# Kernel tuning notes

Hardware: AMD Instinct MI355X
Metric: run time of the kernel (lower is better)

Reference implementation:

```python
import jax, jax.numpy as jnp
import numpy as np

B, S, E = 4, 2048, 512
H, D = 8, 64  # n_head, attn_dim


def setup_inputs() -> dict:
    key = jax.random.key(0)
    ks = jax.random.split(key, 12)
    scale = 0.02
    return {
        "input_q": jax.random.normal(ks[0], (B, S, E), dtype=jnp.float32),
        "input_k": jax.random.normal(ks[1], (B, S, E), dtype=jnp.float32),
        "input_v": jax.random.normal(ks[2], (B, S, E), dtype=jnp.float32),
        "mask": jax.random.randint(ks[3], (B, S, S), 0, 2, dtype=jnp.int32),
        "wq": jax.random.normal(ks[4], (E, H * D), dtype=jnp.float32) * scale,
        "bq": jnp.zeros((H * D,), dtype=jnp.float32),
        "wk": jax.random.normal(ks[5], (E, H * D), dtype=jnp.float32) * scale,
        "bk": jnp.zeros((H * D,), dtype=jnp.float32),
        "wv": jax.random.normal(ks[6], (E, H * D), dtype=jnp.float32) * scale,
        "bv": jnp.zeros((H * D,), dtype=jnp.float32),
        "wo": jax.random.normal(ks[7], (H * D, E), dtype=jnp.float32) * scale,
        "bo": jnp.zeros((E,), dtype=jnp.float32),
    }


def reference(input_q, input_k, input_v, mask, wq, bq, wk, bk, wv, bv, wo, bo):
    b, lq, _ = input_q.shape
    lk = input_k.shape[1]
    # projections -> [b, len, H, D] -> [b, H, len, D]
    q = (input_q @ wq + bq).reshape(b, lq, H, D).transpose(0, 2, 1, 3)
    k = (input_k @ wk + bk).reshape(b, lk, H, D).transpose(0, 2, 1, 3)
    v = (input_v @ wv + bv).reshape(b, lk, H, D).transpose(0, 2, 1, 3)
    # raw scores [b, H, lq, lk]
    score = jnp.einsum("bhqd,bhkd->bhqk", q, k)
    # NOTE: original masks with -1e9 BEFORE dividing by sqrt(attn_dim)
    score = jnp.where(mask[:, None, :, :] == 0, jnp.float32(-1e9), score)
    attn = jax.nn.softmax(score / jnp.sqrt(jnp.float32(D)), axis=-1)
    out = jnp.einsum("bhqk,bhkd->bqhd", attn, v).reshape(b, lq, H * D)
    return out @ wo + bo
```

## Files before the change

kernel.cpp:

```cpp
#include <hip/hip_runtime.h>
#include <hip/hip_bf16.h>
#include <hip/hip_fp16.h>
#include <stdint.h>

#define Bc 4
#define Sc 2048
#define Ec 512
#define Hc 8
#define Dc 64
#define HDc 512

typedef __attribute__((ext_vector_type(8))) short bf16x8;
typedef __attribute__((ext_vector_type(4))) _Float16 f16x4;
typedef __attribute__((ext_vector_type(8))) _Float16 f16x8;
typedef __attribute__((ext_vector_type(4))) float f32x4;
typedef unsigned int u32;

__device__ __forceinline__ unsigned short f2bf(float x) {
    union { float f; unsigned u; } v; v.f = x;
    unsigned r = v.u + 0x7FFFu + ((v.u >> 16) & 1u);
    return (unsigned short)(r >> 16);
}

__device__ __forceinline__ unsigned pkbf2(float a, float b) {
    float2 f; f.x = a; f.y = b;
    __hip_bfloat162 h = __float22bfloat162_rn(f);
    union { __hip_bfloat162 h2; unsigned u; } u; u.h2 = h;
    return u.u;
}

__device__ __forceinline__ unsigned short f2h(float x) {
    return __half_as_ushort(__float2half_rn(x));
}

__device__ __forceinline__ unsigned pkh2(float a, float b) {
    union { __half2 h2; unsigned u; } u;
    u.h2 = __floats2half2_rn(a, b);
    return u.u;
}

__device__ __forceinline__ uint4 pack8(float4 a, float4 b) {
    uint4 v;
    v.x = pkbf2(a.x, a.y); v.y = pkbf2(a.z, a.w);
    v.z = pkbf2(b.x, b.y); v.w = pkbf2(b.z, b.w);
    return v;
}

__device__ __forceinline__ void gload_lds(const void* g, void* l) {
    __builtin_amdgcn_global_load_lds(
        (const __attribute__((address_space(1))) u32*)g,
        (__attribute__((address_space(3))) u32*)l,
        16, 0, 0);
}

__device__ __forceinline__ int vperm(int mt, int c) {
    return ((c >> 2) << 4) + ((mt >> 1) << 3) + ((mt & 1) << 2) + (c & 3);
}

__global__ __launch_bounds__(256) void prep(
    const int* __restrict__ mask, unsigned long long* __restrict__ bits,
    const float* __restrict__ W0, const float* __restrict__ W1,
    const float* __restrict__ W2, const float* __restrict__ W3,
    unsigned short* __restrict__ Wt,
    const float* __restrict__ Xq, const float* __restrict__ Xk,
    const float* __restrict__ Xv, unsigned short* __restrict__ Xb)
{
    const int blk = blockIdx.x;
    __shared__ float t[64][65];
    if (blk < 256) {
        const int z = blk >> 6;
        const float* W = z == 0 ? W0 : (z == 1 ? W1 : (z == 2 ? W2 : W3));
        unsigned short* O = Wt + (size_t)z * Ec * HDc;
        const int k0 = ((blk >> 3) & 7) * 64, n0 = (blk & 7) * 64;
#pragma unroll
        for (int i = 0; i < 16; i++) {
            int idx = threadIdx.x + 256 * i;
            int kr = idx >> 6, nc = idx & 63;
            t[nc][kr] = W[(size_t)(k0 + kr) * HDc + n0 + nc];
        }
        __syncthreads();
#pragma unroll
        for (int i = 0; i < 16; i++) {
            int idx = threadIdx.x + 256 * i;
            int nr = idx >> 6, kc = idx & 63;
            O[(size_t)(n0 + nr) * Ec + k0 + kc] = f2bf(t[nr][kc]);
        }
    } else if (blk < 2304) {
        const int lane = threadIdx.x & 63;
        int wave = ((blk - 256) * 256 + (int)threadIdx.x) >> 6;
        const int nwaves = (2048 * 256) >> 6;
        const int nwords = (Bc * Sc * Sc) / 64;
        for (int w = wave; w < nwords; w += nwaves) {
            int m = mask[(size_t)w * 64 + lane];
            unsigned long long b = __ballot(m != 0);
            if (lane == 0) bits[w] = b;
        }
    } else {
        const int zi = blk - 2304;
        const int z = zi >> 11, wi = zi & 2047;
        const float* X = z == 0 ? Xq : (z == 1 ? Xk : Xv);
        const size_t off = ((size_t)wi * 256 + threadIdx.x) * 8;
        const float4* p = (const float4*)(X + off);
        float4 f0 = p[0], f1 = p[1];
        *(uint4*)(Xb + (size_t)z * 4194304 + off) = pack8(f0, f1);
    }
}

__global__ __launch_bounds__(256) void proj_gemm(
    const unsigned short* __restrict__ Xb, const unsigned short* __restrict__ Wt,
    const float* __restrict__ bq, const float* __restrict__ bk, const float* __restrict__ bv,
    unsigned short* __restrict__ Oq, unsigned short* __restrict__ Ok,
    unsigned short* __restrict__ Vt)
{
    const int z = blockIdx.z;
    const unsigned short* Xz = Xb + (size_t)z * 4194304;
    const unsigned short* Bt = Wt + (size_t)z * Ec * HDc;
    const float* bias = z == 0 ? bq : (z == 1 ? bk : bv);

    const int n0 = blockIdx.x * 128;
    const int m0 = blockIdx.y * 128;
    const int tid = threadIdx.x, lane = tid & 63, w = tid >> 6;
    const int c = lane & 15, quad = lane >> 4;
    const int wm = w & 1, wn = w >> 1;

    __shared__ unsigned short As[128 * 64];
    __shared__ unsigned short Bs[128 * 64];

    f32x4 acc[4][4];
#pragma unroll
    for (int i = 0; i < 4; i++)
#pragma unroll
        for (int j = 0; j < 4; j++) acc[i][j] = (f32x4){0.f, 0.f, 0.f, 0.f};

    for (int k0 = 0; k0 < Ec; k0 += 64) {
        __syncthreads();
#pragma unroll
        for (int jj = 0; jj < 4; jj++) {
            int rb = w * 32 + jj * 8;
            int row = rb + (lane >> 3);
            int dg = (lane & 7) ^ (row & 7);
            gload_lds(Bt + (size_t)(n0 + row) * Ec + k0 + dg * 8, &Bs[rb * 64]);
            gload_lds(Xz + (size_t)(m0 + row) * Ec + k0 + dg * 8, &As[rb * 64]);
        }
        __syncthreads();
#pragma unroll
        for (int ks = 0; ks < 2; ks++) {
            int kg = ks * 4 + quad;
            bf16x8 af[4], bfr[4];
#pragma unroll
            for (int mt = 0; mt < 4; mt++) {
                int row = wm * 64 + mt * 16 + c;
                af[mt] = *(const bf16x8*)&As[row * 64 + ((kg ^ (row & 7)) * 8)];
            }
#pragma unroll
            for (int nt = 0; nt < 4; nt++) {
                int row = wn * 64 + nt * 16 + c;
                bfr[nt] = *(const bf16x8*)&Bs[row * 64 + ((kg ^ (row & 7)) * 8)];
            }
            if (z < 2) {
#pragma unroll
                for (int mt = 0; mt < 4; mt++)
#pragma unroll
                    for (int nt = 0; nt < 4; nt++)
                        acc[mt][nt] = __builtin_amdgcn_mfma_f32_16x16x32_bf16(af[mt], bfr[nt], acc[mt][nt], 0, 0, 0);
            } else {
#pragma unroll
                for (int mt = 0; mt < 4; mt++)
#pragma unroll
                    for (int nt = 0; nt < 4; nt++)
                        acc[mt][nt] = __builtin_amdgcn_mfma_f32_16x16x32_bf16(bfr[nt], af[mt], acc[mt][nt], 0, 0, 0);
            }
        }
    }

    if (z < 2) {
        unsigned short* O = z == 0 ? Oq : Ok;
        const float qs = z == 0 ? 0.125f : 1.0f;
#pragma unroll
        for (int mt = 0; mt < 4; mt++)
#pragma unroll
            for (int r = 0; r < 4; r++) {
                int gm = m0 + wm * 64 + mt * 16 + quad * 4 + r;
#pragma unroll
                for (int nt = 0; nt < 4; nt++) {
                    int gn = n0 + wn * 64 + nt * 16 + c;
                    O[(size_t)gm * HDc + gn] = f2bf((acc[mt][nt][r] + bias[gn]) * qs);
                }
            }
    } else {
#pragma unroll
        for (int mt = 0; mt < 4; mt++) {
            int gm = m0 + wm * 64 + mt * 16 + c;
            int bb = gm >> 11, sPos = gm & (Sc - 1);
            int tbase = (sPos & ~63) + vperm(mt, c);
#pragma unroll
            for (int nt = 0; nt < 4; nt++)
#pragma unroll
                for (int r = 0; r < 4; r++) {
                    int ng = n0 + wn * 64 + nt * 16 + quad * 4 + r;
                    int hh = ng >> 6, d = ng & 63;
                    Vt[((size_t)(bb * Hc + hh) * Dc + d) * Sc + tbase] = f2h(acc[mt][nt][r] + bias[ng]);
                }
        }
    }
}

__global__ __launch_bounds__(128, 2) void attn_kernel(
    const unsigned short* __restrict__ Qb, const unsigned short* __restrict__ Kb,
    const unsigned short* __restrict__ Vt, const unsigned long long* __restrict__ Mb,
    unsigned short* __restrict__ Ob)
{
    const int qt = blockIdx.x;
    const int h  = blockIdx.y;
    const int b  = blockIdx.z;
    const int q0 = qt * 64;
    const int tid = threadIdx.x, lane = tid & 63, w = tid >> 6;
    const int c = lane & 15, quad = lane >> 4;

    __shared__ unsigned short Ks[2][64 * 64];
    __shared__ unsigned short Vs[2][64 * 64];

    const int q_g0 = q0 + w * 32 + c;
    const int q_g1 = q_g0 + 16;
    const size_t qoff0 = ((size_t)b * Sc + q_g0) * HDc + h * Dc;
    const size_t qoff1 = ((size_t)b * Sc + q_g1) * HDc + h * Dc;

    bf16x8 qf0[2], qf1[2];
#pragma unroll
    for (int ks = 0; ks < 2; ks++) {
        qf0[ks] = *(const bf16x8*)(Qb + qoff0 + ks * 32 + quad * 8);
        qf1[ks] = *(const bf16x8*)(Qb + qoff1 + ks * 32 + quad * 8);
    }

    const unsigned long long* mr0 = Mb + ((size_t)b * Sc + q_g0) * (Sc / 64);
    const unsigned long long* mr1 = Mb + ((size_t)b * Sc + q_g1) * (Sc / 64);
    const size_t kbase = ((size_t)b * Sc) * HDc + h * Dc;
    const size_t vbase = ((size_t)(b * Hc + h)) * Dc * Sc;

    f32x4 o0[4], o1[4], osum0, osum1;
#pragma unroll
    for (int i = 0; i < 4; i++) { o0[i] = (f32x4){0.f,0.f,0.f,0.f}; o1[i] = (f32x4){0.f,0.f,0.f,0.f}; }
    osum0 = (f32x4){0.f, 0.f, 0.f, 0.f};
    osum1 = (f32x4){0.f, 0.f, 0.f, 0.f};

    const f16x4 ones = {(_Float16)1.0f, (_Float16)1.0f, (_Float16)1.0f, (_Float16)1.0f};

    auto stage = [&](int kt, int buf) {
#pragma unroll
        for (int j = 0; j < 4; j++) {
            int rb = w * 32 + j * 8;
            int row = rb + (lane >> 3);
            int dg = (lane & 7) ^ (row & 7);
            gload_lds(Kb + kbase + (size_t)(kt * 64 + row) * HDc + dg * 8, &Ks[buf][rb * 64]);
            gload_lds(Vt + vbase + (size_t)row * Sc + kt * 64 + dg * 8, &Vs[buf][rb * 64]);
        }
    };

    stage(0, 0);
    for (int kt = 0; kt < Sc / 64; kt++) {
        const int cur = kt & 1;
        unsigned long long mw0 = mr0[kt];
        unsigned long long mw1 = mr1[kt];
        __syncthreads();
        if (kt + 1 < Sc / 64) stage(kt + 1, cur ^ 1);

        f32x4 s0[4], s1[4];
#pragma unroll
        for (int nt = 0; nt < 4; nt++) { s0[nt] = (f32x4){0.f,0.f,0.f,0.f}; s1[nt] = (f32x4){0.f,0.f,0.f,0.f}; }
#pragma unroll
        for (int ks = 0; ks < 2; ks++) {
            int kg = ks * 4 + quad;
#pragma unroll
            for (int nt = 0; nt < 4; nt++) {
                int t = nt * 16 + c;
                bf16x8 a = *(const bf16x8*)&Ks[cur][t * 64 + ((kg ^ (t & 7)) * 8)];
                s0[nt] = __builtin_amdgcn_mfma_f32_16x16x32_bf16(a, qf0[ks], s0[nt], 0, 0, 0);
                s1[nt] = __builtin_amdgcn_mfma_f32_16x16x32_bf16(a, qf1[ks], s1[nt], 0, 0, 0);
            }
        }

        u32 mlo0 = (u32)(mw0) >> (quad * 4), mhi0 = (u32)(mw0 >> 32) >> (quad * 4);
        u32 mlo1 = (u32)(mw1) >> (quad * 4), mhi1 = (u32)(mw1 >> 32) >> (quad * 4);
        f16x4 pb0[4], pb1[4];
#pragma unroll
        for (int nt = 0; nt < 4; nt++) {
            u32 ms0 = (nt < 2) ? mlo0 : mhi0;
            u32 ms1 = (nt < 2) ? mlo1 : mhi1;
            float p0[4], p1[4];
#pragma unroll
            for (int r = 0; r < 4; r++) {
                const int sh = (nt & 1) * 16 + r;
                int k0 = ((int)(ms0 << (31 - sh))) >> 31;
                int k1 = ((int)(ms1 << (31 - sh))) >> 31;
                p0[r] = __int_as_float(__float_as_int(__expf(s0[nt][r])) & k0);
                p1[r] = __int_as_float(__float_as_int(__expf(s1[nt][r])) & k1);
            }
            union { unsigned u[2]; f16x4 v; } pk;
            pk.u[0] = pkh2(p0[0], p0[1]); pk.u[1] = pkh2(p0[2], p0[3]);
            pb0[nt] = pk.v;
            pk.u[0] = pkh2(p1[0], p1[1]); pk.u[1] = pkh2(p1[2], p1[3]);
            pb1[nt] = pk.v;
        }

#pragma unroll
        for (int a = 0; a < 2; a++) {
#pragma unroll
            for (int dt = 0; dt < 4; dt++) {
                int d = dt * 16 + c;
                union { f16x8 v8; f16x4 v4[2]; } vv;
                vv.v8 = *(const f16x8*)&Vs[cur][d * 64 + (((quad * 2 + a) ^ (d & 7)) * 8)];
                o0[dt] = __builtin_amdgcn_mfma_f32_16x16x16f16(vv.v4[0], pb0[2*a],   o0[dt], 0, 0, 0);
                o0[dt] = __builtin_amdgcn_mfma_f32_16x16x16f16(vv.v4[1], pb0[2*a+1], o0[dt], 0, 0, 0);
                o1[dt] = __builtin_amdgcn_mfma_f32_16x16x16f16(vv.v4[0], pb1[2*a],   o1[dt], 0, 0, 0);
                o1[dt] = __builtin_amdgcn_mfma_f32_16x16x16f16(vv.v4[1], pb1[2*a+1], o1[dt], 0, 0, 0);
            }
            osum0 = __builtin_amdgcn_mfma_f32_16x16x16f16(ones, pb0[2*a],   osum0, 0, 0, 0);
            osum0 = __builtin_amdgcn_mfma_f32_16x16x16f16(ones, pb0[2*a+1], osum0, 0, 0, 0);
            osum1 = __builtin_amdgcn_mfma_f32_16x16x16f16(ones, pb1[2*a],   osum1, 0, 0, 0);
            osum1 = __builtin_amdgcn_mfma_f32_16x16x16f16(ones, pb1[2*a+1], osum1, 0, 0, 0);
        }
    }

    const float inv0 = 1.0f / osum0[0];
    const float inv1 = 1.0f / osum1[0];

#pragma unroll
    for (int dt = 0; dt < 4; dt++) {
        uint2 pk;
        pk.x = pkbf2(o0[dt][0] * inv0, o0[dt][1] * inv0);
        pk.y = pkbf2(o0[dt][2] * inv0, o0[dt][3] * inv0);
        *(uint2*)(Ob + qoff0 + dt * 16 + quad * 4) = pk;
        pk.x = pkbf2(o1[dt][0] * inv1, o1[dt][1] * inv1);
        pk.y = pkbf2(o1[dt][2] * inv1, o1[dt][3] * inv1);
        *(uint2*)(Ob + qoff1 + dt * 16 + quad * 4) = pk;
    }
}

__global__ __launch_bounds__(256) void out_gemm(
    const unsigned short* __restrict__ Ab, const unsigned short* __restrict__ Bt,
    const float* __restrict__ bias, float* __restrict__ Out)
{
    const int n0 = blockIdx.x * 128;
    const int m0 = blockIdx.y * 64;
    const int tid = threadIdx.x, lane = tid & 63, w = tid >> 6;
    const int c = lane & 15, quad = lane >> 4;
    const int wm = w & 1, wn = w >> 1;

    __shared__ unsigned short As[64 * 64];
    __shared__ unsigned short Bs[128 * 64];

    f32x4 acc[2][4];
#pragma unroll
    for (int i = 0; i < 2; i++)
#pragma unroll
        for (int j = 0; j < 4; j++) acc[i][j] = (f32x4){0.f, 0.f, 0.f, 0.f};

    for (int k0 = 0; k0 < HDc; k0 += 64) {
        __syncthreads();
#pragma unroll
        for (int jj = 0; jj < 4; jj++) {
            int rb = w * 32 + jj * 8;
            int row = rb + (lane >> 3);
            int dg = (lane & 7) ^ (row & 7);
            gload_lds(Bt + (size_t)(n0 + row) * Ec + k0 + dg * 8, &Bs[rb * 64]);
        }
#pragma unroll
        for (int jj = 0; jj < 2; jj++) {
            int rb = w * 16 + jj * 8;
            int row = rb + (lane >> 3);
            int dg = (lane & 7) ^ (row & 7);
            gload_lds(Ab + (size_t)(m0 + row) * HDc + k0 + dg * 8, &As[rb * 64]);
        }
        __syncthreads();
#pragma unroll
        for (int ks = 0; ks < 2; ks++) {
            int kg = ks * 4 + quad;
            bf16x8 af[2], bfr[4];
#pragma unroll
            for (int mt = 0; mt < 2; mt++) {
                int row = wm * 32 + mt * 16 + c;
                af[mt] = *(const bf16x8*)&As[row * 64 + ((kg ^ (row & 7)) * 8)];
            }
#pragma unroll
            for (int nt = 0; nt < 4; nt++) {
                int row = wn * 64 + nt * 16 + c;
                bfr[nt] = *(const bf16x8*)&Bs[row * 64 + ((kg ^ (row & 7)) * 8)];
            }
#pragma unroll
            for (int mt = 0; mt < 2; mt++)
#pragma unroll
                for (int nt = 0; nt < 4; nt++)
                    acc[mt][nt] = __builtin_amdgcn_mfma_f32_16x16x32_bf16(af[mt], bfr[nt], acc[mt][nt], 0, 0, 0);
        }
    }
#pragma unroll
    for (int mt = 0; mt < 2; mt++)
#pragma unroll
        for (int r = 0; r < 4; r++) {
            int gm = m0 + wm * 32 + mt * 16 + quad * 4 + r;
#pragma unroll
            for (int nt = 0; nt < 4; nt++) {
                int gn = n0 + wn * 64 + nt * 16 + c;
                Out[(size_t)gm * Ec + gn] = acc[mt][nt][r] + bias[gn];
            }
        }
}

extern "C" void kernel_launch(void* const* d_in, const int* in_sizes, int n_in,
                              void* d_out, int out_size, void* d_ws, size_t ws_size,
                              hipStream_t stream)
{
    const float* xq = (const float*)d_in[0];
    const float* xk = (const float*)d_in[1];
    const float* xv = (const float*)d_in[2];
    const int* mask = (const int*)d_in[3];
    const float* wq = (const float*)d_in[4];
    const float* bq = (const float*)d_in[5];
    const float* wk = (const float*)d_in[6];
    const float* bk = (const float*)d_in[7];
    const float* wv = (const float*)d_in[8];
    const float* bv = (const float*)d_in[9];
    const float* wo = (const float*)d_in[10];
    const float* bo = (const float*)d_in[11];
    float* out = (float*)d_out;

    char* ws = (char*)d_ws;
    const size_t MB = 1024 * 1024;
    unsigned short* qb = (unsigned short*)(ws + 0 * MB);
    unsigned short* kb = (unsigned short*)(ws + 8 * MB);
    unsigned short* vt = (unsigned short*)(ws + 16 * MB);
    unsigned short* xb = (unsigned short*)(ws + 24 * MB);
    unsigned short* ab = (unsigned short*)(ws + 24 * MB);
    unsigned long long* mb = (unsigned long long*)(ws + 48 * MB);
    unsigned short* wt = (unsigned short*)(ws + 50 * MB);

    hipLaunchKernelGGL(prep, dim3(8448), dim3(256), 0, stream,
                       mask, mb, wq, wk, wv, wo, wt, xq, xk, xv, xb);

    hipLaunchKernelGGL(proj_gemm, dim3(4, 64, 3), dim3(256), 0, stream,
                       xb, wt, bq, bk, bv, qb, kb, vt);

    hipLaunchKernelGGL(attn_kernel, dim3(32, 8, 4), dim3(128), 0, stream,
                       qb, kb, vt, mb, ab);

    hipLaunchKernelGGL(out_gemm, dim3(4, 128), dim3(256), 0, stream,
                       ab, wt + 3 * (size_t)Ec * HDc, bo, out);
}
```

Baseline: 292.2 us.

## Widen attention blocks to 128 queries and pipeline QK^T one tile ahead

The attention kernel now runs 4 waves per block covering 128 query rows, so each staged K/V tile is shared by twice as many waves and the grid is halved. K/V staging moves to a triple-buffered ring. The score MFMAs for tile kt+1 are computed while the softmax and PV work for tile kt proceeds, with a single barrier at the end of each iteration. This is meant to hide LDS and global latency behind MFMA work and cut K/V load traffic. The cost is extra live score registers and more shared memory, which may reduce occupancy. The end-of-iteration barrier may also drain the just-issued prefetch, limiting the overlap.

```diff
diff --git a/kernel.cpp b/kernel.cpp
--- a/kernel.cpp
+++ b/kernel.cpp
@@ -15,6 +15,7 @@
 typedef __attribute__((ext_vector_type(8))) _Float16 f16x8;
 typedef __attribute__((ext_vector_type(4))) float f32x4;
 typedef unsigned int u32;
+typedef unsigned long long u64;
 
 __device__ __forceinline__ unsigned short f2bf(float x) {
     union { float f; unsigned u; } v; v.f = x;
@@ -205,7 +206,7 @@
     }
 }
 
-__global__ __launch_bounds__(128, 2) void attn_kernel(
+__global__ __launch_bounds__(256, 2) void attn_kernel(
     const unsigned short* __restrict__ Qb, const unsigned short* __restrict__ Kb,
     const unsigned short* __restrict__ Vt, const unsigned long long* __restrict__ Mb,
     unsigned short* __restrict__ Ob)
@@ -213,17 +214,17 @@
     const int qt = blockIdx.x;
     const int h  = blockIdx.y;
     const int b  = blockIdx.z;
-    const int q0 = qt * 64;
+    const int q0 = qt * 128;
     const int tid = threadIdx.x, lane = tid & 63, w = tid >> 6;
     const int c = lane & 15, quad = lane >> 4;
 
-    __shared__ unsigned short Ks[2][64 * 64];
-    __shared__ unsigned short Vs[2][64 * 64];
-
-    const int q_g0 = q0 + w * 32 + c;
-    const int q_g1 = q_g0 + 16;
-    const size_t qoff0 = ((size_t)b * Sc + q_g0) * HDc + h * Dc;
-    const size_t qoff1 = ((size_t)b * Sc + q_g1) * HDc + h * Dc;
+    __shared__ unsigned short Ks[3][64 * 64];
+    __shared__ unsigned short Vs[3][64 * 64];
+
+    const int qg0 = q0 + w * 32 + c;
+    const int qg1 = qg0 + 16;
+    const size_t qoff0 = ((size_t)b * Sc + qg0) * HDc + h * Dc;
+    const size_t qoff1 = ((size_t)b * Sc + qg1) * HDc + h * Dc;
 
     bf16x8 qf0[2], qf1[2];
 #pragma unroll
@@ -232,8 +233,8 @@
         qf1[ks] = *(const bf16x8*)(Qb + qoff1 + ks * 32 + quad * 8);
     }
 
-    const unsigned long long* mr0 = Mb + ((size_t)b * Sc + q_g0) * (Sc / 64);
-    const unsigned long long* mr1 = Mb + ((size_t)b * Sc + q_g1) * (Sc / 64);
+    const unsigned long long* mr0 = Mb + ((size_t)b * Sc + qg0) * (Sc / 64);
+    const unsigned long long* mr1 = Mb + ((size_t)b * Sc + qg1) * (Sc / 64);
     const size_t kbase = ((size_t)b * Sc) * HDc + h * Dc;
     const size_t vbase = ((size_t)(b * Hc + h)) * Dc * Sc;
 
@@ -247,8 +248,8 @@
 
     auto stage = [&](int kt, int buf) {
 #pragma unroll
-        for (int j = 0; j < 4; j++) {
-            int rb = w * 32 + j * 8;
+        for (int j = 0; j < 2; j++) {
+            int rb = w * 16 + j * 8;
             int row = rb + (lane >> 3);
             int dg = (lane & 7) ^ (row & 7);
             gload_lds(Kb + kbase + (size_t)(kt * 64 + row) * HDc + dg * 8, &Ks[buf][rb * 64]);
@@ -256,28 +257,38 @@
         }
     };
 
+    auto computeS = [&](const unsigned short* kb2, f32x4* s0, f32x4* s1) {
+#pragma unroll
+        for (int nt = 0; nt < 4; nt++) { s0[nt] = (f32x4){0.f,0.f,0.f,0.f}; s1[nt] = (f32x4){0.f,0.f,0.f,0.f}; }
+#pragma unroll
+        for (int ks = 0; ks < 2; ks++) {
+            int kg = ks * 4 + quad;
+#pragma unroll
+            for (int nt = 0; nt < 4; nt++) {
+                int t = nt * 16 + c;
+                bf16x8 a = *(const bf16x8*)&kb2[t * 64 + ((kg ^ (t & 7)) * 8)];
+                s0[nt] = __builtin_amdgcn_mfma_f32_16x16x32_bf16(a, qf0[ks], s0[nt], 0, 0, 0);
+                s1[nt] = __builtin_amdgcn_mfma_f32_16x16x32_bf16(a, qf1[ks], s1[nt], 0, 0, 0);
+            }
+        }
+    };
+
+    f32x4 sA0[4], sA1[4];
+
     stage(0, 0);
+    stage(1, 1);
+    __syncthreads();
+    computeS(Ks[0], sA0, sA1);
+
+    int cur = 0, nxt = 1, stg = 2;
     for (int kt = 0; kt < Sc / 64; kt++) {
-        const int cur = kt & 1;
         unsigned long long mw0 = mr0[kt];
         unsigned long long mw1 = mr1[kt];
-        __syncthreads();
-        if (kt + 1 < Sc / 64) stage(kt + 1, cur ^ 1);
-
-        f32x4 s0[4], s1[4];
-#pragma unroll
-        for (int nt = 0; nt < 4; nt++) { s0[nt] = (f32x4){0.f,0.f,0.f,0.f}; s1[nt] = (f32x4){0.f,0.f,0.f,0.f}; }
-#pragma unroll
-        for (int ks = 0; ks < 2; ks++) {
-            int kg = ks * 4 + quad;
-#pragma unroll
-            for (int nt = 0; nt < 4; nt++) {
-                int t = nt * 16 + c;
-                bf16x8 a = *(const bf16x8*)&Ks[cur][t * 64 + ((kg ^ (t & 7)) * 8)];
-                s0[nt] = __builtin_amdgcn_mfma_f32_16x16x32_bf16(a, qf0[ks], s0[nt], 0, 0, 0);
-                s1[nt] = __builtin_amdgcn_mfma_f32_16x16x32_bf16(a, qf1[ks], s1[nt], 0, 0, 0);
-            }
-        }
+
+        if (kt + 2 < Sc / 64) stage(kt + 2, stg);
+
+        f32x4 sB0[4], sB1[4];
+        if (kt + 1 < Sc / 64) computeS(Ks[nxt], sB0, sB1);
 
         u32 mlo0 = (u32)(mw0) >> (quad * 4), mhi0 = (u32)(mw0 >> 32) >> (quad * 4);
         u32 mlo1 = (u32)(mw1) >> (quad * 4), mhi1 = (u32)(mw1 >> 32) >> (quad * 4);
@@ -292,8 +303,8 @@
                 const int sh = (nt & 1) * 16 + r;
                 int k0 = ((int)(ms0 << (31 - sh))) >> 31;
                 int k1 = ((int)(ms1 << (31 - sh))) >> 31;
-                p0[r] = __int_as_float(__float_as_int(__expf(s0[nt][r])) & k0);
-                p1[r] = __int_as_float(__float_as_int(__expf(s1[nt][r])) & k1);
+                p0[r] = __int_as_float(__float_as_int(__expf(sA0[nt][r])) & k0);
+                p1[r] = __int_as_float(__float_as_int(__expf(sA1[nt][r])) & k1);
             }
             union { unsigned u[2]; f16x4 v; } pk;
             pk.u[0] = pkh2(p0[0], p0[1]); pk.u[1] = pkh2(p0[2], p0[3]);
@@ -302,13 +313,14 @@
             pb1[nt] = pk.v;
         }
 
+        const unsigned short* vb = Vs[cur];
 #pragma unroll
         for (int a = 0; a < 2; a++) {
 #pragma unroll
             for (int dt = 0; dt < 4; dt++) {
                 int d = dt * 16 + c;
                 union { f16x8 v8; f16x4 v4[2]; } vv;
-                vv.v8 = *(const f16x8*)&Vs[cur][d * 64 + (((quad * 2 + a) ^ (d & 7)) * 8)];
+                vv.v8 = *(const f16x8*)&vb[d * 64 + (((quad * 2 + a) ^ (d & 7)) * 8)];
                 o0[dt] = __builtin_amdgcn_mfma_f32_16x16x16f16(vv.v4[0], pb0[2*a],   o0[dt], 0, 0, 0);
                 o0[dt] = __builtin_amdgcn_mfma_f32_16x16x16f16(vv.v4[1], pb0[2*a+1], o0[dt], 0, 0, 0);
                 o1[dt] = __builtin_amdgcn_mfma_f32_16x16x16f16(vv.v4[0], pb1[2*a],   o1[dt], 0, 0, 0);
@@ -319,6 +331,12 @@
             osum1 = __builtin_amdgcn_mfma_f32_16x16x16f16(ones, pb1[2*a],   osum1, 0, 0, 0);
             osum1 = __builtin_amdgcn_mfma_f32_16x16x16f16(ones, pb1[2*a+1], osum1, 0, 0, 0);
         }
+
+        __syncthreads();
+
+#pragma unroll
+        for (int i = 0; i < 4; i++) { sA0[i] = sB0[i]; sA1[i] = sB1[i]; }
+        int t = cur; cur = nxt; nxt = stg; stg = t;
     }
 
     const float inv0 = 1.0f / osum0[0];
@@ -440,7 +458,7 @@
     hipLaunchKernelGGL(proj_gemm, dim3(4, 64, 3), dim3(256), 0, stream,
                        xb, wt, bq, bk, bv, qb, kb, vt);
 
-    hipLaunchKernelGGL(attn_kernel, dim3(32, 8, 4), dim3(128), 0, stream,
+    hipLaunchKernelGGL(attn_kernel, dim3(16, 8, 4), dim3(256), 0, stream,
                        qb, kb, vt, mb, ab);
 
     hipLaunchKernelGGL(out_gemm, dim3(4, 128), dim3(256), 0, stream,
```

Result: faster. 279.6 us (-4.3%).
